# Kernel tuning notes

Hardware: AMD Instinct MI355X
Metric: run time of the kernel (lower is better)

## Reference

```python
import jax, jax.numpy as jnp
import numpy as np
import math

B, S, D, H = 2, 2048, 1024, 16
DH = D // H          # 64 head dim
BLK = 64             # SpargeAttn block size
TOPK = 0.5           # fraction of KV blocks kept per query block
NEG = -1e9


def setup_inputs() -> dict:
    key = jax.random.key(0)
    ks = jax.random.split(key, 8)
    s = 0.02
    return {
        "inputs": jax.random.normal(ks[0], (B, S, D), dtype=jnp.float32),
        "ln_g": jnp.ones((D,), jnp.float32),
        "ln_b": jnp.zeros((D,), jnp.float32),
        "Wq": jax.random.normal(ks[1], (D, D), jnp.float32) * s,
        "bq": jnp.zeros((D,), jnp.float32),
        "Wk": jax.random.normal(ks[2], (D, D), jnp.float32) * s,
        "bk": jnp.zeros((D,), jnp.float32),
        "Wv": jax.random.normal(ks[3], (D, D), jnp.float32) * s,
        "bv": jnp.zeros((D,), jnp.float32),
        "Wo": jax.random.normal(ks[4], (D, D), jnp.float32) * s,
        "bo": jnp.zeros((D,), jnp.float32),
    }


def _sparse_topk_attn(q, k, v):
    # q,k,v: [B,H,S,DH]. Block-mean-similarity top-k sparse causal attention
    # (SpargeAttn spas_sage2_attn_meansim_topk, fp32 reference semantics).
    nb = S // BLK
    qm = q.reshape(B, H, nb, BLK, DH).mean(3)          # [B,H,nb,DH]
    km = k.reshape(B, H, nb, BLK, DH).mean(3)
    sim = jnp.einsum('bhqd,bhkd->bhqk', qm, km)        # block similarity
    cblk = jnp.tril(jnp.ones((nb, nb), bool))          # causal block mask
    sim = jnp.where(cblk, sim, NEG)
    kk = max(1, int(math.ceil(TOPK * nb)))
    _, idx = jax.lax.top_k(sim, kk)                    # [B,H,nb,kk]
    blk = jax.nn.one_hot(idx, nb, dtype=jnp.float32).sum(-2) > 0  # [B,H,nb,nb]
    blk = (blk & cblk) | jnp.eye(nb, dtype=bool)       # keep diagonal block
    tok_mask = jnp.repeat(jnp.repeat(blk, BLK, axis=2), BLK, axis=3)  # [B,H,S,S]
    tok_mask = tok_mask & jnp.tril(jnp.ones((S, S), bool))
    scores = jnp.einsum('bhid,bhjd->bhij', q, k) / jnp.float32(math.sqrt(DH))
    scores = jnp.where(tok_mask, scores, NEG)
    p = jax.nn.softmax(scores, axis=-1)
    return jnp.einsum('bhij,bhjd->bhid', p, v)


def reference(inputs, ln_g, ln_b, Wq, bq, Wk, bk, Wv, bv, Wo, bo):
    # pre-norm LayerNorm
    mu = inputs.mean(-1, keepdims=True)
    var = inputs.var(-1, keepdims=True)
    x = (inputs - mu) * jax.lax.rsqrt(var + 1e-5) * ln_g + ln_b
    # QKV projections -> [B,H,S,DH]
    q = (x @ Wq + bq).reshape(B, S, H, DH).transpose(0, 2, 1, 3)
    k = (x @ Wk + bk).reshape(B, S, H, DH).transpose(0, 2, 1, 3)
    v = (x @ Wv + bv).reshape(B, S, H, DH).transpose(0, 2, 1, 3)
    ctx = _sparse_topk_attn(q, k, v)
    ctx = ctx.transpose(0, 2, 1, 3).reshape(B, S, D)
    return ctx @ Wo + bo
```

## Files before the change

### kernel.cpp

```cpp
#include <hip/hip_runtime.h>
#include <stdint.h>

#define DEV static __device__ __forceinline__

typedef __attribute__((ext_vector_type(8))) short s16x8;
typedef __attribute__((ext_vector_type(4))) float f32x4;

constexpr int Bdim = 2, Sdim = 2048, Ddim = 1024, Hdim = 16, DH = 64;
constexpr int Mrows = Bdim * Sdim;
constexpr int NB = 32;
constexpr int SEL_STRIDE = 18;

#define QSCALE 0.18033688011112042f
#define MFIX   8.0f

constexpr size_t OFF_XB    = 0;
constexpr size_t OFF_WTQKV = OFF_XB    + (size_t)Mrows*Ddim*2;
constexpr size_t OFF_WOT   = OFF_WTQKV + (size_t)3072*1024*2;
constexpr size_t OFF_QKV   = OFF_WOT   + (size_t)1024*1024*2;
constexpr size_t OFF_CTX   = OFF_QKV   + (size_t)Mrows*3072*2;
constexpr size_t OFF_XM    = OFF_CTX   + (size_t)Mrows*Ddim*2;
constexpr size_t OFF_QM    = OFF_XM    + (size_t)64*1024*4;
constexpr size_t OFF_KM    = OFF_QM    + (size_t)64*1024*4;
constexpr size_t OFF_BIASQ = OFF_KM    + (size_t)64*1024*4;
constexpr size_t OFF_SEL   = OFF_BIASQ + (size_t)3072*4;
constexpr size_t OFF_PART  = OFF_SEL   + (size_t)1024*SEL_STRIDE*4;

DEV float bf2f(unsigned short u){ union{unsigned int i; float f;} x; x.i = ((unsigned int)u)<<16; return x.f; }
DEV unsigned short f2bf(float f){ union{float f; unsigned int i;} x; x.f=f;
  unsigned int r = x.i + 0x7fffu + ((x.i>>16)&1u); return (unsigned short)(r>>16); }

DEV void gload16(const unsigned short* g, unsigned short* l){
  __builtin_amdgcn_global_load_lds(
      (__attribute__((address_space(1))) void*)(void*)g,
      (__attribute__((address_space(3))) void*)l, 16, 0, 0);
}

DEV unsigned int cvtpk(float a, float b){
  unsigned int r;
  asm("v_cvt_pk_bf16_f32 %0, %1, %2" : "=v"(r) : "v"(a), "v"(b));
  return r;
}

DEV float exp2fast(float x){
  float r;
  asm("v_exp_f32 %0, %1" : "=v"(r) : "v"(x));
  return r;
}

__global__ __launch_bounds__(256) void ln_kernel(const float* __restrict__ inp,
                                                 const float* __restrict__ gam,
                                                 const float* __restrict__ bet,
                                                 unsigned short* __restrict__ xb){
  const int row = blockIdx.x, t = threadIdx.x;
  __shared__ float red[8];
  const float4 v = ((const float4*)(inp + (size_t)row*Ddim))[t];
  float s  = v.x + v.y + v.z + v.w;
  float s2 = v.x*v.x + v.y*v.y + v.z*v.z + v.w*v.w;
#pragma unroll
  for (int mk=32; mk>=1; mk>>=1){ s += __shfl_xor(s, mk); s2 += __shfl_xor(s2, mk); }
  if ((t&63)==0){ red[t>>6] = s; red[4+(t>>6)] = s2; }
  __syncthreads();
  s  = red[0]+red[1]+red[2]+red[3];
  s2 = red[4]+red[5]+red[6]+red[7];
  const float mu  = s * (1.f/Ddim);
  const float var = s2 * (1.f/Ddim) - mu*mu;
  const float rs  = rsqrtf(var + 1e-5f);
  const float4 gv = ((const float4*)gam)[t];
  const float4 bv = ((const float4*)bet)[t];
  float o0 = (v.x-mu)*rs*gv.x + bv.x;
  float o1 = (v.y-mu)*rs*gv.y + bv.y;
  float o2 = (v.z-mu)*rs*gv.z + bv.z;
  float o3 = (v.w-mu)*rs*gv.w + bv.w;
  uint2 u;
  u.x = (unsigned int)f2bf(o0) | ((unsigned int)f2bf(o1)<<16);
  u.y = (unsigned int)f2bf(o2) | ((unsigned int)f2bf(o3)<<16);
  ((uint2*)(xb + (size_t)row*Ddim))[t] = u;
}

__global__ __launch_bounds__(256) void xm_kernel(const float* __restrict__ inp,
                                                 const float* __restrict__ gam,
                                                 const float* __restrict__ bet,
                                                 float* __restrict__ xm){
  const int blk = blockIdx.x, t = threadIdx.x;
  const int w = t>>6, lane = t&63;
  __shared__ float part[4][1024];
  float4 gv[4], bv[4];
#pragma unroll
  for (int p=0;p<4;++p){ gv[p] = ((const float4*)gam)[lane + 64*p];
                         bv[p] = ((const float4*)bet)[lane + 64*p]; }
  float ax[4][4];
#pragma unroll
  for (int p=0;p<4;++p)
#pragma unroll
    for (int c=0;c<4;++c) ax[p][c]=0.f;
  for (int rr=0; rr<16; ++rr){
    const int row = blk*64 + w*16 + rr;
    const float4* rp = (const float4*)(inp + (size_t)row*Ddim);
    float4 v[4]; float s=0.f, s2=0.f;
#pragma unroll
    for (int p=0;p<4;++p){
      v[p] = rp[lane + 64*p];
      s  += v[p].x+v[p].y+v[p].z+v[p].w;
      s2 += v[p].x*v[p].x+v[p].y*v[p].y+v[p].z*v[p].z+v[p].w*v[p].w;
    }
#pragma unroll
    for (int mk=32; mk>=1; mk>>=1){ s += __shfl_xor(s,mk); s2 += __shfl_xor(s2,mk); }
    const float mu = s*(1.f/Ddim);
    const float var = s2*(1.f/Ddim) - mu*mu;
    const float rs = rsqrtf(var + 1e-5f);
#pragma unroll
    for (int p=0;p<4;++p){
      ax[p][0] += (v[p].x-mu)*rs*gv[p].x + bv[p].x;
      ax[p][1] += (v[p].y-mu)*rs*gv[p].y + bv[p].y;
      ax[p][2] += (v[p].z-mu)*rs*gv[p].z + bv[p].z;
      ax[p][3] += (v[p].w-mu)*rs*gv[p].w + bv[p].w;
    }
  }
#pragma unroll
  for (int p=0;p<4;++p){
    float4 o; o.x=ax[p][0]; o.y=ax[p][1]; o.z=ax[p][2]; o.w=ax[p][3];
    ((float4*)&part[w][0])[lane + 64*p] = o;
  }
  __syncthreads();
  float4 r0 = ((float4*)&part[0][0])[t];
  float4 r1 = ((float4*)&part[1][0])[t];
  float4 r2 = ((float4*)&part[2][0])[t];
  float4 r3 = ((float4*)&part[3][0])[t];
  float4 o;
  o.x = (r0.x+r1.x+r2.x+r3.x)*(1.f/64);
  o.y = (r0.y+r1.y+r2.y+r3.y)*(1.f/64);
  o.z = (r0.z+r1.z+r2.z+r3.z)*(1.f/64);
  o.w = (r0.w+r1.w+r2.w+r3.w)*(1.f/64);
  ((float4*)(xm + (size_t)blk*Ddim))[t] = o;
}

__global__ __launch_bounds__(256) void wtrans4_kernel(const float* __restrict__ Wq,
                                                      const float* __restrict__ Wk,
                                                      const float* __restrict__ Wv,
                                                      const float* __restrict__ Wo,
                                                      const float* __restrict__ bq,
                                                      const float* __restrict__ bk,
                                                      const float* __restrict__ bv,
                                                      unsigned short* __restrict__ wtqkv,
                                                      unsigned short* __restrict__ wot,
                                                      float* __restrict__ bqkv){
  __shared__ float tile[32][33];
  const int z = blockIdx.z;
  const float* W = (z==0)?Wq:(z==1)?Wk:(z==2)?Wv:Wo;
  unsigned short* Wt = (z<3) ? (wtqkv + (size_t)z*1024*1024) : wot;
  const int n0 = blockIdx.x*32, k0 = blockIdx.y*32;
  const int t = threadIdx.x, r = t>>5, c = t&31;
  if (z<3 && blockIdx.x==0 && blockIdx.y==0){
    const float* bb = (z==0)?bq:(z==1)?bk:bv;
#pragma unroll
    for (int i=0;i<4;++i) bqkv[z*1024 + t + 256*i] = bb[t + 256*i];
  }
#pragma unroll
  for (int i=0;i<4;++i) tile[r+8*i][c] = W[(size_t)(k0 + r + 8*i)*1024 + n0 + c];
  __syncthreads();
  const int nr = t >> 3, kq = (t & 7) * 4;
  unsigned int w0 = (unsigned int)f2bf(tile[kq  ][nr]) | ((unsigned int)f2bf(tile[kq+1][nr])<<16);
  unsigned int w1 = (unsigned int)f2bf(tile[kq+2][nr]) | ((unsigned int)f2bf(tile[kq+3][nr])<<16);
  uint2 st; st.x = w0; st.y = w1;
  *(uint2*)&Wt[(size_t)(n0 + nr)*1024 + k0 + kq] = st;
}

__global__ __launch_bounds__(256) void qmkm_part(const float* __restrict__ xm,
    const float* __restrict__ Wq, const float* __restrict__ Wk,
    float* __restrict__ part){
  const int c  = blockIdx.x*256 + threadIdx.x;
  const int rg = blockIdx.y >> 3, ks = blockIdx.y & 7;
  const int z  = blockIdx.z;
  const float* W = z ? Wk : Wq;
  const int r0 = rg*16, k0 = ks*128;
  float acc[16];
#pragma unroll
  for (int r=0;r<16;++r) acc[r]=0.f;
  for (int k=0;k<128;k+=4){
    const float wv0 = W[(size_t)(k0+k  )*1024 + c];
    const float wv1 = W[(size_t)(k0+k+1)*1024 + c];
    const float wv2 = W[(size_t)(k0+k+2)*1024 + c];
    const float wv3 = W[(size_t)(k0+k+3)*1024 + c];
#pragma unroll
    for (int r=0;r<16;++r){
      const float4 xv = *(const float4*)&xm[(size_t)(r0+r)*1024 + k0 + k];
      acc[r] = fmaf(xv.w, wv3, fmaf(xv.z, wv2, fmaf(xv.y, wv1, fmaf(xv.x, wv0, acc[r]))));
    }
  }
  float* dst = part + (((size_t)z*8 + ks)*64 + r0)*1024 + c;
#pragma unroll
  for (int r=0;r<16;++r) dst[(size_t)r*1024] = acc[r];
}

__global__ __launch_bounds__(256) void qmkm_reduce(const float* __restrict__ part,
    const float* __restrict__ bq, const float* __restrict__ bk,
    float* __restrict__ qm, float* __restrict__ km){
  const int idx = blockIdx.x*256 + threadIdx.x;
  const int z = blockIdx.y;
  const int c = idx & 1023, r = idx >> 10;
  const float* p = part + ((size_t)z*8*64*1024) + (size_t)r*1024 + c;
  float s = 0.f;
#pragma unroll
  for (int ks=0; ks<8; ++ks) s += p[(size_t)ks*64*1024];
  s += z ? bk[c] : bq[c];
  (z ? km : qm)[(size_t)r*1024 + c] = s;
}

__global__ __launch_bounds__(256) void topk_kernel(const float* __restrict__ qm,
                                                   const float* __restrict__ km,
                                                   int* __restrict__ sel){
  const int bhq = blockIdx.x;
  const int qb = bhq & 31, h = (bhq>>5) & 15, b = bhq >> 9;
  const int t = threadIdx.x;
  __shared__ float sim[32];
  __shared__ int keep[32];
  const int kb = t>>3, l8 = t&7;
  float acc = 0.f;
  if (kb <= qb){
    const float* qv = qm + (size_t)(b*32 + qb)*1024 + h*64;
    const float* kv = km + (size_t)(b*32 + kb)*1024 + h*64;
#pragma unroll
    for (int d=0; d<8; ++d) acc += qv[l8*8+d] * kv[l8*8+d];
  }
  acc += __shfl_xor(acc,1); acc += __shfl_xor(acc,2); acc += __shfl_xor(acc,4);
  if (l8==0) sim[kb] = (kb<=qb) ? acc : -1e30f;
  __syncthreads();
  if (t < 32){
    int k2 = t; int ok = 0;
    if (k2 <= qb){
      float sv = sim[k2]; int rank = 0;
      for (int j=0;j<=qb;++j){
        float sj = sim[j];
        rank += (sj > sv) || (sj == sv && j < k2);
      }
      ok = (rank < 16) || (k2 == qb);
    }
    keep[t] = ok;
  }
  __syncthreads();
  if (t == 0){
    int* dstp = sel + (size_t)bhq * SEL_STRIDE;
    int c = 0;
    for (int j=0;j<32;++j) if (keep[j]) dstp[1+c++] = j;
    dstp[0] = c;
  }
}

#define G_STAGE(bsel, kofs) do { \
  gload16(A0 + (kofs), ldsA + (bsel)*4096 + (wid*2+0)*512); \
  gload16(A1 + (kofs), ldsA + (bsel)*4096 + (wid*2+1)*512); \
  gload16(B0 + (kofs), ldsB + (bsel)*4096 + (wid*2+0)*512); \
  gload16(B1 + (kofs), ldsB + (bsel)*4096 + (wid*2+1)*512); \
} while(0)

#define G_COMPUTE(bsel) do { \
  s16x8 af[4], bfr[4]; \
  _Pragma("unroll") \
  for (int mi=0;mi<4;++mi){ \
    int row = wr*64 + mi*16 + rl; \
    af[mi] = *(const s16x8*)((char*)ldsA + (bsel)*8192 + row*64 + ((g ^ ((row>>1)&3))<<4)); \
  } \
  _Pragma("unroll") \
  for (int ni=0;ni<4;++ni){ \
    int row = wc*64 + ni*16 + rl; \
    bfr[ni] = *(const s16x8*)((char*)ldsB + (bsel)*8192 + row*64 + ((g ^ ((row>>1)&3))<<4)); \
  } \
  _Pragma("unroll") \
  for (int mi=0;mi<4;++mi) \
    _Pragma("unroll") \
    for (int ni=0;ni<4;++ni) \
      acc[mi][ni] = __builtin_amdgcn_mfma_f32_16x16x32_bf16(af[mi], bfr[ni], acc[mi][ni], 0,0,0); \
} while(0)

template<int OUT_BF16, int SCALEQ>
__global__ __launch_bounds__(256) void gemm_bt(const unsigned short* __restrict__ A,
                                               const unsigned short* __restrict__ Bt,
                                               const float* __restrict__ bias,
                                               void* __restrict__ C, int N){
  constexpr int K = 1024;
  constexpr int NT = K/32;
  __shared__ unsigned short ldsA[3*128*32];
  __shared__ unsigned short ldsB[3*128*32];
  const int t = threadIdx.x, lane = t & 63, wid = t >> 6;
  const int wr = wid >> 1, wc = wid & 1;
  const int rl = lane & 15, g = lane >> 4;

  const int nbx = gridDim.x, nby = gridDim.y;
  const int id  = blockIdx.y * nbx + blockIdx.x;
  const int xcd = id & 7, j = id >> 3;
  const int MBP = nby >> 2, NBP = nbx >> 1;
  const int mg = xcd >> 1, ng = xcd & 1;
  const int m0 = (mg*MBP + (j % MBP)) * 128;
  const int n0 = (ng*NBP + (j / MBP)) * 128;

  const f32x4 ZERO4 = {0.f,0.f,0.f,0.f};
  f32x4 acc[4][4];
#pragma unroll
  for (int i=0;i<4;++i)
#pragma unroll
    for (int j2=0;j2<4;++j2) acc[i][j2] = ZERO4;

  const int slot0 = wid*128 + lane, slot1 = slot0 + 64;
  const int sr0 = slot0>>2, sc0 = slot0&3;
  const int sr1 = slot1>>2, sc1 = slot1&3;
  const unsigned short* A0 = A  + (size_t)(m0 + sr0)*K + (sc0 ^ ((sr0>>1)&3))*8;
  const unsigned short* A1 = A  + (size_t)(m0 + sr1)*K + (sc1 ^ ((sr1>>1)&3))*8;
  const unsigned short* B0 = Bt + (size_t)(n0 + sr0)*K + (sc0 ^ ((sr0>>1)&3))*8;
  const unsigned short* B1 = Bt + (size_t)(n0 + sr1)*K + (sc1 ^ ((sr1>>1)&3))*8;

  G_STAGE(0, 0);
  G_STAGE(1, 32);

  for (int ti=0; ti<NT; ++ti){
    const int cur = ti % 3;
    if (ti+2 < NT){
      G_STAGE((ti+2)%3, (ti+2)*32);
      asm volatile("s_waitcnt vmcnt(8)" ::: "memory");
    } else if (ti+1 < NT){
      asm volatile("s_waitcnt vmcnt(4)" ::: "memory");
    } else {
      asm volatile("s_waitcnt vmcnt(0)" ::: "memory");
    }
    __builtin_amdgcn_s_barrier();
    __builtin_amdgcn_sched_barrier(0);
    G_COMPUTE(cur);
    __builtin_amdgcn_sched_barrier(0);
    __builtin_amdgcn_s_barrier();
  }

  const int r4 = g*4;
#pragma unroll
  for (int mi=0;mi<4;++mi){
#pragma unroll
    for (int ni=0;ni<4;++ni){
      int col = n0 + wc*64 + ni*16 + rl;
      float bb = bias[col];
      float sc = (SCALEQ && col < 1024) ? QSCALE : 1.0f;
#pragma unroll
      for (int e=0;e<4;++e){
        int row = m0 + wr*64 + mi*16 + r4 + e;
        float v = (acc[mi][ni][e] + bb) * sc;
        if (OUT_BF16) ((unsigned short*)C)[(size_t)row*N + col] = f2bf(v);
        else          ((float*)C)[(size_t)row*N + col] = v;
      }
    }
  }
}

#define G64_STAGE(bsel, kofs) do { \
  gload16(A0 + (kofs), ldsA + (bsel)*4096 + (wid*2+0)*512); \
  gload16(A1 + (kofs), ldsA + (bsel)*4096 + (wid*2+1)*512); \
  gload16(B0 + (kofs), ldsB + (bsel)*2048 + wid*512); \
} while(0)

#define G64_COMPUTE(bsel) do { \
  s16x8 af[4], bfr[2]; \
  _Pragma("unroll") \
  for (int mi=0;mi<4;++mi){ \
    int row = wr*64 + mi*16 + rl; \
    af[mi] = *(const s16x8*)((char*)ldsA + (bsel)*8192 + row*64 + ((g ^ ((row>>1)&3))<<4)); \
  } \
  _Pragma("unroll") \
  for (int ni=0;ni<2;++ni){ \
    int row = wc*32 + ni*16 + rl; \
    bfr[ni] = *(const s16x8*)((char*)ldsB + (bsel)*4096 + row*64 + ((g ^ ((row>>1)&3))<<4)); \
  } \
  _Pragma("unroll") \
  for (int mi=0;mi<4;++mi) \
    _Pragma("unroll") \
    for (int ni=0;ni<2;++ni) \
      acc[mi][ni] = __builtin_amdgcn_mfma_f32_16x16x32_bf16(af[mi], bfr[ni], acc[mi][ni], 0,0,0); \
} while(0)

__global__ __launch_bounds__(256) void gemm_bt64(const unsigned short* __restrict__ A,
                                                 const unsigned short* __restrict__ Bt,
                                                 const float* __restrict__ bias,
                                                 float* __restrict__ C, int N){
  constexpr int K = 1024;
  constexpr int NT = K/32;
  __shared__ unsigned short ldsA[3*128*32];
  __shared__ unsigned short ldsB[3*64*32];
  const int t = threadIdx.x, lane = t & 63, wid = t >> 6;
  const int wr = wid >> 1, wc = wid & 1;
  const int rl = lane & 15, g = lane >> 4;

  const int id  = blockIdx.y * gridDim.x + blockIdx.x;
  const int xcd = id & 7, j = id >> 3;
  const int mg = xcd >> 1, ng = xcd & 1;
  const int m0 = (mg*8 + (j & 7)) * 128;
  const int n0 = (ng*8 + (j >> 3)) * 64;

  const f32x4 ZERO4 = {0.f,0.f,0.f,0.f};
  f32x4 acc[4][2];
#pragma unroll
  for (int i=0;i<4;++i)
#pragma unroll
    for (int j2=0;j2<2;++j2) acc[i][j2] = ZERO4;

  const int slot0 = wid*128 + lane, slot1 = slot0 + 64;
  const int sr0 = slot0>>2, sc0 = slot0&3;
  const int sr1 = slot1>>2, sc1 = slot1&3;
  const unsigned short* A0 = A + (size_t)(m0 + sr0)*K + (sc0 ^ ((sr0>>1)&3))*8;
  const unsigned short* A1 = A + (size_t)(m0 + sr1)*K + (sc1 ^ ((sr1>>1)&3))*8;
  const int slotB = wid*64 + lane;
  const int srB = slotB>>2, scB = slotB&3;
  const unsigned short* B0 = Bt + (size_t)(n0 + srB)*K + (scB ^ ((srB>>1)&3))*8;

  G64_STAGE(0, 0);
  G64_STAGE(1, 32);

  for (int ti=0; ti<NT; ++ti){
    const int cur = ti % 3;
    if (ti+2 < NT){
      G64_STAGE((ti+2)%3, (ti+2)*32);
      asm volatile("s_waitcnt vmcnt(6)" ::: "memory");
    } else if (ti+1 < NT){
      asm volatile("s_waitcnt vmcnt(3)" ::: "memory");
    } else {
      asm volatile("s_waitcnt vmcnt(0)" ::: "memory");
    }
    __builtin_amdgcn_s_barrier();
    __builtin_amdgcn_sched_barrier(0);
    G64_COMPUTE(cur);
    __builtin_amdgcn_sched_barrier(0);
    __builtin_amdgcn_s_barrier();
  }

  const int r4 = g*4;
#pragma unroll
  for (int mi=0;mi<4;++mi){
#pragma unroll
    for (int ni=0;ni<2;++ni){
      int col = n0 + wc*32 + ni*16 + rl;
      float bb = bias[col];
#pragma unroll
      for (int e=0;e<4;++e){
        int row = m0 + wr*64 + mi*16 + r4 + e;
        C[(size_t)row*N + col] = acc[mi][ni][e] + bb;
      }
    }
  }
}

__global__ __launch_bounds__(256) void attn_kernel(const unsigned short* __restrict__ qkv,
                                                   const int* __restrict__ sel,
                                                   unsigned short* __restrict__ ctx){
  const int id = blockIdx.x;
  const int xcd = id & 7, jj = id >> 3;
  const int bh = xcd + 8*(jj/24);
  const int tau = jj % 24;
  const int h = bh & 15, b = bh >> 4;
  int qbl[2]; int nq;
  if (tau < 8){ qbl[0]=tau; qbl[1]=15-tau; nq=2; }
  else        { qbl[0]=tau+8; qbl[1]=0;    nq=1; }

  const int t = threadIdx.x, wid = t >> 6, lane = t & 63;
  const int rl = lane & 15, g = lane >> 4;
  const int q_local = wid*16 + rl;

  __shared__ unsigned short K_s[2][4096];
  __shared__ unsigned short V_s[2][4096];

  const int jst = t >> 2, cq = t & 3;
  const int r2 = t >> 3, dq = t & 7;
  const unsigned short* kbase = qkv + (size_t)(b*Sdim + jst)*3072 + 1024 + h*DH + cq*16;
  const unsigned short* vbase = qkv + (size_t)(b*Sdim + 2*r2)*3072 + 2048 + h*DH + dq*8;
  const int kwb0 = jst*128 + (((cq*2  ) ^ (jst&7))<<4);
  const int kwb1 = jst*128 + (((cq*2+1) ^ (jst&7))<<4);
  const f32x4 ZERO4 = {0.f,0.f,0.f,0.f};

  const int src0 = (rl + 16*((2*g  ) & 3)) << 2;
  const int src1 = (rl + 16*((2*g+1) & 3)) << 2;
  const bool hsel = (g >> 1);

  for (int iq=0; iq<nq; ++iq){
    const int qb = qbl[iq];
    const int* selrow = sel + (size_t)(((b*Hdim)+h)*NB + qb) * SEL_STRIDE;
    const int ns = selrow[0];

    const int qg0 = b*Sdim + qb*64 + q_local;
    const unsigned short* qbase = qkv + (size_t)qg0*3072 + h*DH;
    s16x8 qa[2];
    qa[0] = *(const s16x8*)(qbase + g*8);
    qa[1] = *(const s16x8*)(qbase + 32 + g*8);

    f32x4 o[4];
    float l_p = 0.f;
#pragma unroll
    for (int f=0; f<4; ++f) o[f] = ZERO4;

    __syncthreads();

    int kb = selrow[1];
    s16x8 kr0, kr1, vr0, vr1;
    {
      const size_t off = (size_t)kb*64*3072;
      kr0 = *(const s16x8*)(kbase + off);
      kr1 = *(const s16x8*)(kbase + off + 8);
      vr0 = *(const s16x8*)(vbase + off);
      vr1 = *(const s16x8*)(vbase + off + 3072);
    }

    for (int it=0; it<ns; ++it){
      const int buf = it & 1;
      unsigned short* Kw = &K_s[buf][0];
      unsigned short* Vw = &V_s[buf][0];
      *(s16x8*)((char*)Kw + kwb0) = kr0;
      *(s16x8*)((char*)Kw + kwb1) = kr1;
#pragma unroll
      for (int e=0;e<8;++e){
        const int d1 = dq*8 + e;
        const int sw = (d1&7) ^ (d1>>3);
        const unsigned int pr = (unsigned int)(unsigned short)vr0[e]
                              | ((unsigned int)(unsigned short)vr1[e] << 16);
        *(unsigned int*)((char*)Vw + d1*128 + ((4*r2) ^ (sw<<4))) = pr;
      }
      const int kbcur = kb;
      if (it+1 < ns){
        kb = selrow[2+it];
        const size_t off = (size_t)kb*64*3072;
        kr0 = *(const s16x8*)(kbase + off);
        kr1 = *(const s16x8*)(kbase + off + 8);
        vr0 = *(const s16x8*)(vbase + off);
        vr1 = *(const s16x8*)(vbase + off + 3072);
      }
      __syncthreads();

      f32x4 sfT[4];
#pragma unroll
      for (int f=0;f<4;++f) sfT[f] = ZERO4;
      __builtin_amdgcn_s_setprio(1);
#pragma unroll
      for (int kk=0;kk<2;++kk){
#pragma unroll
        for (int f=0;f<4;++f){
          const int jr = f*16 + rl;
          s16x8 kf = *(const s16x8*)((char*)Kw + jr*128 + (((kk*4+g) ^ (jr&7))<<4));
          sfT[f] = __builtin_amdgcn_mfma_f32_16x16x32_bf16(kf, qa[kk], sfT[f], 0,0,0);
        }
      }
      __builtin_amdgcn_s_setprio(0);
      if (kbcur == qb){
#pragma unroll
        for (int f=0;f<4;++f)
#pragma unroll
          for (int e=0;e<4;++e){
            const int j2 = f*16 + g*4 + e;
            if (j2 > q_local) sfT[f][e] = -1e9f;
          }
      }
      {
        float rs = 0.f;
#pragma unroll
        for (int f=0;f<4;++f)
#pragma unroll
          for (int e=0;e<4;++e){
            const float p = exp2fast(sfT[f][e] - MFIX);
            sfT[f][e] = p; rs += p;
          }
        l_p += rs;
      }

      unsigned int plo[4], phi[4];
#pragma unroll
      for (int f=0;f<4;++f){
        plo[f] = cvtpk(sfT[f][0], sfT[f][1]);
        phi[f] = cvtpk(sfT[f][2], sfT[f][3]);
      }

#pragma unroll
      for (int kk=0;kk<2;++kk){
        const int f0 = 2*kk, f1 = 2*kk+1;
        unsigned int a0, b0, w0, w1, w2, w3;
        a0 = __builtin_amdgcn_ds_bpermute(src0, plo[f0]);
        b0 = __builtin_amdgcn_ds_bpermute(src0, plo[f1]);
        w0 = hsel ? b0 : a0;
        a0 = __builtin_amdgcn_ds_bpermute(src0, phi[f0]);
        b0 = __builtin_amdgcn_ds_bpermute(src0, phi[f1]);
        w1 = hsel ? b0 : a0;
        a0 = __builtin_amdgcn_ds_bpermute(src1, plo[f0]);
        b0 = __builtin_amdgcn_ds_bpermute(src1, plo[f1]);
        w2 = hsel ? b0 : a0;
        a0 = __builtin_amdgcn_ds_bpermute(src1, phi[f0]);
        b0 = __builtin_amdgcn_ds_bpermute(src1, phi[f1]);
        w3 = hsel ? b0 : a0;
        union { unsigned int u[4]; s16x8 v; } pfc;
        pfc.u[0] = w0; pfc.u[1] = w1; pfc.u[2] = w2; pfc.u[3] = w3;
        const s16x8 pf = pfc.v;
        __builtin_amdgcn_s_setprio(1);
#pragma unroll
        for (int f=0;f<4;++f){
          const int d = f*16 + rl;
          const int sw = (d&7) ^ (d>>3);
          s16x8 vf = *(const s16x8*)((char*)Vw + d*128 + ((64*kk + 16*g) ^ (sw<<4)));
          o[f] = __builtin_amdgcn_mfma_f32_16x16x32_bf16(vf, pf, o[f], 0,0,0);
        }
        __builtin_amdgcn_s_setprio(0);
      }
    }

    {
      float l_r = l_p;
      l_r += __shfl_xor(l_r, 16);
      l_r += __shfl_xor(l_r, 32);
      const float inv = 1.f / l_r;
      unsigned short* crow = ctx + (size_t)qg0*Ddim + h*DH;
#pragma unroll
      for (int f=0;f<4;++f){
        uint2 st;
        st.x = (unsigned int)f2bf(o[f][0]*inv) | ((unsigned int)f2bf(o[f][1]*inv)<<16);
        st.y = (unsigned int)f2bf(o[f][2]*inv) | ((unsigned int)f2bf(o[f][3]*inv)<<16);
        *(uint2*)(crow + f*16 + g*4) = st;
      }
    }
  }
}

extern "C" void kernel_launch(void* const* d_in, const int* in_sizes, int n_in,
                              void* d_out, int out_size, void* d_ws, size_t ws_size,
                              hipStream_t stream){
  (void)in_sizes; (void)n_in; (void)out_size; (void)ws_size;
  const float* inp  = (const float*)d_in[0];
  const float* ln_g = (const float*)d_in[1];
  const float* ln_b = (const float*)d_in[2];
  const float* Wq   = (const float*)d_in[3];
  const float* bq   = (const float*)d_in[4];
  const float* Wk   = (const float*)d_in[5];
  const float* bk   = (const float*)d_in[6];
  const float* Wv   = (const float*)d_in[7];
  const float* bv   = (const float*)d_in[8];
  const float* Wo   = (const float*)d_in[9];
  const float* bo   = (const float*)d_in[10];

  char* ws = (char*)d_ws;
  unsigned short* xb    = (unsigned short*)(ws + OFF_XB);
  unsigned short* wtqkv = (unsigned short*)(ws + OFF_WTQKV);
  unsigned short* wot   = (unsigned short*)(ws + OFF_WOT);
  unsigned short* qkvb  = (unsigned short*)(ws + OFF_QKV);
  unsigned short* ctx   = (unsigned short*)(ws + OFF_CTX);
  float* xm   = (float*)(ws + OFF_XM);
  float* qm   = (float*)(ws + OFF_QM);
  float* km   = (float*)(ws + OFF_KM);
  float* bqkv = (float*)(ws + OFF_BIASQ);
  int*   sel  = (int*)(ws + OFF_SEL);
  float* part = (float*)(ws + OFF_PART);

  ln_kernel<<<Mrows, 256, 0, stream>>>(inp, ln_g, ln_b, xb);
  xm_kernel<<<64, 256, 0, stream>>>(inp, ln_g, ln_b, xm);
  wtrans4_kernel<<<dim3(32,32,4), 256, 0, stream>>>(Wq, Wk, Wv, Wo, bq, bk, bv, wtqkv, wot, bqkv);
  qmkm_part<<<dim3(4,32,2), 256, 0, stream>>>(xm, Wq, Wk, part);
  qmkm_reduce<<<dim3(256,2), 256, 0, stream>>>(part, bq, bk, qm, km);
  topk_kernel<<<1024, 256, 0, stream>>>(qm, km, sel);
  gemm_bt<1,1><<<dim3(24,32), 256, 0, stream>>>(xb, wtqkv, bqkv, (void*)qkvb, 3072);
  attn_kernel<<<768, 256, 0, stream>>>(qkvb, sel, ctx);
  gemm_bt64<<<dim3(16,32), 256, 0, stream>>>(ctx, wot, bo, (float*)d_out, 1024);
}
```

Baseline: 140.0 us.

## Fuse LN, block-mean and weight transpose kernels; one query block per attention CTA

Merges the layernorm, block-mean and weight transpose/convert kernels into one prep kernel that picks its role from the block index, cutting two launches and letting the three jobs overlap on the GPU. The attention kernel now gives each CTA a single query block (1024 CTAs), launched with the heaviest causal query blocks first, replacing the old pairing of two query blocks per CTA. Finer work units may balance load better and shorten the tail, at the cost of more CTAs and less reuse of setup work. The fused prep kernel always reserves 16 KB of shared memory, which may lower occupancy for the layernorm blocks.

New measurement: 141.3 us. Within noise of the previous version (+0.9%).

```diff
diff --git a/kernel.cpp b/kernel.cpp
--- a/kernel.cpp
+++ b/kernel.cpp
@@ -48,122 +48,124 @@
   return r;
 }
 
-__global__ __launch_bounds__(256) void ln_kernel(const float* __restrict__ inp,
-                                                 const float* __restrict__ gam,
-                                                 const float* __restrict__ bet,
-                                                 unsigned short* __restrict__ xb){
-  const int row = blockIdx.x, t = threadIdx.x;
-  __shared__ float red[8];
-  const float4 v = ((const float4*)(inp + (size_t)row*Ddim))[t];
-  float s  = v.x + v.y + v.z + v.w;
-  float s2 = v.x*v.x + v.y*v.y + v.z*v.z + v.w*v.w;
-#pragma unroll
-  for (int mk=32; mk>=1; mk>>=1){ s += __shfl_xor(s, mk); s2 += __shfl_xor(s2, mk); }
-  if ((t&63)==0){ red[t>>6] = s; red[4+(t>>6)] = s2; }
-  __syncthreads();
-  s  = red[0]+red[1]+red[2]+red[3];
-  s2 = red[4]+red[5]+red[6]+red[7];
-  const float mu  = s * (1.f/Ddim);
-  const float var = s2 * (1.f/Ddim) - mu*mu;
-  const float rs  = rsqrtf(var + 1e-5f);
-  const float4 gv = ((const float4*)gam)[t];
-  const float4 bv = ((const float4*)bet)[t];
-  float o0 = (v.x-mu)*rs*gv.x + bv.x;
-  float o1 = (v.y-mu)*rs*gv.y + bv.y;
-  float o2 = (v.z-mu)*rs*gv.z + bv.z;
-  float o3 = (v.w-mu)*rs*gv.w + bv.w;
-  uint2 u;
-  u.x = (unsigned int)f2bf(o0) | ((unsigned int)f2bf(o1)<<16);
-  u.y = (unsigned int)f2bf(o2) | ((unsigned int)f2bf(o3)<<16);
-  ((uint2*)(xb + (size_t)row*Ddim))[t] = u;
-}
-
-__global__ __launch_bounds__(256) void xm_kernel(const float* __restrict__ inp,
-                                                 const float* __restrict__ gam,
-                                                 const float* __restrict__ bet,
-                                                 float* __restrict__ xm){
-  const int blk = blockIdx.x, t = threadIdx.x;
-  const int w = t>>6, lane = t&63;
-  __shared__ float part[4][1024];
-  float4 gv[4], bv[4];
-#pragma unroll
-  for (int p=0;p<4;++p){ gv[p] = ((const float4*)gam)[lane + 64*p];
-                         bv[p] = ((const float4*)bet)[lane + 64*p]; }
-  float ax[4][4];
-#pragma unroll
-  for (int p=0;p<4;++p)
-#pragma unroll
-    for (int c=0;c<4;++c) ax[p][c]=0.f;
-  for (int rr=0; rr<16; ++rr){
-    const int row = blk*64 + w*16 + rr;
-    const float4* rp = (const float4*)(inp + (size_t)row*Ddim);
-    float4 v[4]; float s=0.f, s2=0.f;
+__global__ __launch_bounds__(256) void prep_kernel(const float* __restrict__ inp,
+                                                   const float* __restrict__ gam,
+                                                   const float* __restrict__ bet,
+                                                   const float* __restrict__ Wq,
+                                                   const float* __restrict__ Wk,
+                                                   const float* __restrict__ Wv,
+                                                   const float* __restrict__ Wo,
+                                                   const float* __restrict__ bq,
+                                                   const float* __restrict__ bk,
+                                                   const float* __restrict__ bv,
+                                                   unsigned short* __restrict__ xb,
+                                                   float* __restrict__ xm,
+                                                   unsigned short* __restrict__ wtqkv,
+                                                   unsigned short* __restrict__ wot,
+                                                   float* __restrict__ bqkv){
+  __shared__ float sh[4][1024];
+  const int bid = blockIdx.x;
+  const int t = threadIdx.x;
+
+  if (bid < 4096){
+    const int row = bid;
+    float* red = &sh[0][0];
+    const float4 v = ((const float4*)(inp + (size_t)row*Ddim))[t];
+    float s  = v.x + v.y + v.z + v.w;
+    float s2 = v.x*v.x + v.y*v.y + v.z*v.z + v.w*v.w;
+#pragma unroll
+    for (int mk=32; mk>=1; mk>>=1){ s += __shfl_xor(s, mk); s2 += __shfl_xor(s2, mk); }
+    if ((t&63)==0){ red[t>>6] = s; red[4+(t>>6)] = s2; }
+    __syncthreads();
+    s  = red[0]+red[1]+red[2]+red[3];
+    s2 = red[4]+red[5]+red[6]+red[7];
+    const float mu  = s * (1.f/Ddim);
+    const float var = s2 * (1.f/Ddim) - mu*mu;
+    const float rs  = rsqrtf(var + 1e-5f);
+    const float4 gv = ((const float4*)gam)[t];
+    const float4 bv2 = ((const float4*)bet)[t];
+    float o0 = (v.x-mu)*rs*gv.x + bv2.x;
+    float o1 = (v.y-mu)*rs*gv.y + bv2.y;
+    float o2 = (v.z-mu)*rs*gv.z + bv2.z;
+    float o3 = (v.w-mu)*rs*gv.w + bv2.w;
+    uint2 u;
+    u.x = (unsigned int)f2bf(o0) | ((unsigned int)f2bf(o1)<<16);
+    u.y = (unsigned int)f2bf(o2) | ((unsigned int)f2bf(o3)<<16);
+    ((uint2*)(xb + (size_t)row*Ddim))[t] = u;
+  } else if (bid < 4160){
+    const int blk = bid - 4096;
+    const int w = t>>6, lane = t&63;
+    float4 gv[4], bvv[4];
+#pragma unroll
+    for (int p=0;p<4;++p){ gv[p] = ((const float4*)gam)[lane + 64*p];
+                           bvv[p] = ((const float4*)bet)[lane + 64*p]; }
+    float ax[4][4];
+#pragma unroll
+    for (int p=0;p<4;++p)
+#pragma unroll
+      for (int c=0;c<4;++c) ax[p][c]=0.f;
+    for (int rr=0; rr<16; ++rr){
+      const int row = blk*64 + w*16 + rr;
+      const float4* rp = (const float4*)(inp + (size_t)row*Ddim);
+      float4 v[4]; float s=0.f, s2=0.f;
+#pragma unroll
+      for (int p=0;p<4;++p){
+        v[p] = rp[lane + 64*p];
+        s  += v[p].x+v[p].y+v[p].z+v[p].w;
+        s2 += v[p].x*v[p].x+v[p].y*v[p].y+v[p].z*v[p].z+v[p].w*v[p].w;
+      }
+#pragma unroll
+      for (int mk=32; mk>=1; mk>>=1){ s += __shfl_xor(s,mk); s2 += __shfl_xor(s2,mk); }
+      const float mu = s*(1.f/Ddim);
+      const float var = s2*(1.f/Ddim) - mu*mu;
+      const float rs = rsqrtf(var + 1e-5f);
+#pragma unroll
+      for (int p=0;p<4;++p){
+        ax[p][0] += (v[p].x-mu)*rs*gv[p].x + bvv[p].x;
+        ax[p][1] += (v[p].y-mu)*rs*gv[p].y + bvv[p].y;
+        ax[p][2] += (v[p].z-mu)*rs*gv[p].z + bvv[p].z;
+        ax[p][3] += (v[p].w-mu)*rs*gv[p].w + bvv[p].w;
+      }
+    }
 #pragma unroll
     for (int p=0;p<4;++p){
-      v[p] = rp[lane + 64*p];
-      s  += v[p].x+v[p].y+v[p].z+v[p].w;
-      s2 += v[p].x*v[p].x+v[p].y*v[p].y+v[p].z*v[p].z+v[p].w*v[p].w;
-    }
-#pragma unroll
-    for (int mk=32; mk>=1; mk>>=1){ s += __shfl_xor(s,mk); s2 += __shfl_xor(s2,mk); }
-    const float mu = s*(1.f/Ddim);
-    const float var = s2*(1.f/Ddim) - mu*mu;
-    const float rs = rsqrtf(var + 1e-5f);
-#pragma unroll
-    for (int p=0;p<4;++p){
-      ax[p][0] += (v[p].x-mu)*rs*gv[p].x + bv[p].x;
-      ax[p][1] += (v[p].y-mu)*rs*gv[p].y + bv[p].y;
-      ax[p][2] += (v[p].z-mu)*rs*gv[p].z + bv[p].z;
-      ax[p][3] += (v[p].w-mu)*rs*gv[p].w + bv[p].w;
-    }
-  }
-#pragma unroll
-  for (int p=0;p<4;++p){
-    float4 o; o.x=ax[p][0]; o.y=ax[p][1]; o.z=ax[p][2]; o.w=ax[p][3];
-    ((float4*)&part[w][0])[lane + 64*p] = o;
-  }
-  __syncthreads();
-  float4 r0 = ((float4*)&part[0][0])[t];
-  float4 r1 = ((float4*)&part[1][0])[t];
-  float4 r2 = ((float4*)&part[2][0])[t];
-  float4 r3 = ((float4*)&part[3][0])[t];
-  float4 o;
-  o.x = (r0.x+r1.x+r2.x+r3.x)*(1.f/64);
-  o.y = (r0.y+r1.y+r2.y+r3.y)*(1.f/64);
-  o.z = (r0.z+r1.z+r2.z+r3.z)*(1.f/64);
-  o.w = (r0.w+r1.w+r2.w+r3.w)*(1.f/64);
-  ((float4*)(xm + (size_t)blk*Ddim))[t] = o;
-}
-
-__global__ __launch_bounds__(256) void wtrans4_kernel(const float* __restrict__ Wq,
-                                                      const float* __restrict__ Wk,
-                                                      const float* __restrict__ Wv,
-                                                      const float* __restrict__ Wo,
-                                                      const float* __restrict__ bq,
-                                                      const float* __restrict__ bk,
-                                                      const float* __restrict__ bv,
-                                                      unsigned short* __restrict__ wtqkv,
-                                                      unsigned short* __restrict__ wot,
-                                                      float* __restrict__ bqkv){
-  __shared__ float tile[32][33];
-  const int z = blockIdx.z;
-  const float* W = (z==0)?Wq:(z==1)?Wk:(z==2)?Wv:Wo;
-  unsigned short* Wt = (z<3) ? (wtqkv + (size_t)z*1024*1024) : wot;
-  const int n0 = blockIdx.x*32, k0 = blockIdx.y*32;
-  const int t = threadIdx.x, r = t>>5, c = t&31;
-  if (z<3 && blockIdx.x==0 && blockIdx.y==0){
-    const float* bb = (z==0)?bq:(z==1)?bk:bv;
-#pragma unroll
-    for (int i=0;i<4;++i) bqkv[z*1024 + t + 256*i] = bb[t + 256*i];
-  }
-#pragma unroll
-  for (int i=0;i<4;++i) tile[r+8*i][c] = W[(size_t)(k0 + r + 8*i)*1024 + n0 + c];
-  __syncthreads();
-  const int nr = t >> 3, kq = (t & 7) * 4;
-  unsigned int w0 = (unsigned int)f2bf(tile[kq  ][nr]) | ((unsigned int)f2bf(tile[kq+1][nr])<<16);
-  unsigned int w1 = (unsigned int)f2bf(tile[kq+2][nr]) | ((unsigned int)f2bf(tile[kq+3][nr])<<16);
-  uint2 st; st.x = w0; st.y = w1;
-  *(uint2*)&Wt[(size_t)(n0 + nr)*1024 + k0 + kq] = st;
+      float4 o; o.x=ax[p][0]; o.y=ax[p][1]; o.z=ax[p][2]; o.w=ax[p][3];
+      ((float4*)&sh[w][0])[lane + 64*p] = o;
+    }
+    __syncthreads();
+    float4 r0 = ((float4*)&sh[0][0])[t];
+    float4 r1 = ((float4*)&sh[1][0])[t];
+    float4 r2 = ((float4*)&sh[2][0])[t];
+    float4 r3 = ((float4*)&sh[3][0])[t];
+    float4 o;
+    o.x = (r0.x+r1.x+r2.x+r3.x)*(1.f/64);
+    o.y = (r0.y+r1.y+r2.y+r3.y)*(1.f/64);
+    o.z = (r0.z+r1.z+r2.z+r3.z)*(1.f/64);
+    o.w = (r0.w+r1.w+r2.w+r3.w)*(1.f/64);
+    ((float4*)(xm + (size_t)blk*Ddim))[t] = o;
+  } else {
+    const int wt = bid - 4160;
+    const int z = wt >> 10, rem = wt & 1023;
+    const int bx = rem & 31, by = rem >> 5;
+    const float* W = (z==0)?Wq:(z==1)?Wk:(z==2)?Wv:Wo;
+    unsigned short* Wt = (z<3) ? (wtqkv + (size_t)z*1024*1024) : wot;
+    const int n0 = bx*32, k0 = by*32;
+    const int r = t>>5, c = t&31;
+    float (*tile)[33] = (float(*)[33])&sh[0][0];
+    if (z<3 && bx==0 && by==0){
+      const float* bb = (z==0)?bq:(z==1)?bk:bv;
+#pragma unroll
+      for (int i=0;i<4;++i) bqkv[z*1024 + t + 256*i] = bb[t + 256*i];
+    }
+#pragma unroll
+    for (int i=0;i<4;++i) tile[r+8*i][c] = W[(size_t)(k0 + r + 8*i)*1024 + n0 + c];
+    __syncthreads();
+    const int nr = t >> 3, kq = (t & 7) * 4;
+    unsigned int w0 = (unsigned int)f2bf(tile[kq  ][nr]) | ((unsigned int)f2bf(tile[kq+1][nr])<<16);
+    unsigned int w1 = (unsigned int)f2bf(tile[kq+2][nr]) | ((unsigned int)f2bf(tile[kq+3][nr])<<16);
+    uint2 st; st.x = w0; st.y = w1;
+    *(uint2*)&Wt[(size_t)(n0 + nr)*1024 + k0 + kq] = st;
+  }
 }
 
 __global__ __launch_bounds__(256) void qmkm_part(const float* __restrict__ xm,
@@ -448,12 +450,9 @@
                                                    unsigned short* __restrict__ ctx){
   const int id = blockIdx.x;
   const int xcd = id & 7, jj = id >> 3;
-  const int bh = xcd + 8*(jj/24);
-  const int tau = jj % 24;
+  const int bh = xcd + 8*(jj >> 5);
+  const int qb = 31 - (jj & 31);
   const int h = bh & 15, b = bh >> 4;
-  int qbl[2]; int nq;
-  if (tau < 8){ qbl[0]=tau; qbl[1]=15-tau; nq=2; }
-  else        { qbl[0]=tau+8; qbl[1]=0;    nq=1; }
 
   const int t = threadIdx.x, wid = t >> 6, lane = t & 63;
   const int rl = lane & 15, g = lane >> 4;
@@ -474,145 +473,140 @@
   const int src1 = (rl + 16*((2*g+1) & 3)) << 2;
   const bool hsel = (g >> 1);
 
-  for (int iq=0; iq<nq; ++iq){
-    const int qb = qbl[iq];
-    const int* selrow = sel + (size_t)(((b*Hdim)+h)*NB + qb) * SEL_STRIDE;
-    const int ns = selrow[0];
-
-    const int qg0 = b*Sdim + qb*64 + q_local;
-    const unsigned short* qbase = qkv + (size_t)qg0*3072 + h*DH;
-    s16x8 qa[2];
-    qa[0] = *(const s16x8*)(qbase + g*8);
-    qa[1] = *(const s16x8*)(qbase + 32 + g*8);
-
-    f32x4 o[4];
-    float l_p = 0.f;
-#pragma unroll
-    for (int f=0; f<4; ++f) o[f] = ZERO4;
-
-    __syncthreads();
-
-    int kb = selrow[1];
-    s16x8 kr0, kr1, vr0, vr1;
-    {
+  const int* selrow = sel + (size_t)(((b*Hdim)+h)*NB + qb) * SEL_STRIDE;
+  const int ns = selrow[0];
+
+  const int qg0 = b*Sdim + qb*64 + q_local;
+  const unsigned short* qbase = qkv + (size_t)qg0*3072 + h*DH;
+  s16x8 qa[2];
+  qa[0] = *(const s16x8*)(qbase + g*8);
+  qa[1] = *(const s16x8*)(qbase + 32 + g*8);
+
+  f32x4 o[4];
+  float l_p = 0.f;
+#pragma unroll
+  for (int f=0; f<4; ++f) o[f] = ZERO4;
+
+  int kb = selrow[1];
+  s16x8 kr0, kr1, vr0, vr1;
+  {
+    const size_t off = (size_t)kb*64*3072;
+    kr0 = *(const s16x8*)(kbase + off);
+    kr1 = *(const s16x8*)(kbase + off + 8);
+    vr0 = *(const s16x8*)(vbase + off);
+    vr1 = *(const s16x8*)(vbase + off + 3072);
+  }
+
+  for (int it=0; it<ns; ++it){
+    const int buf = it & 1;
+    unsigned short* Kw = &K_s[buf][0];
+    unsigned short* Vw = &V_s[buf][0];
+    *(s16x8*)((char*)Kw + kwb0) = kr0;
+    *(s16x8*)((char*)Kw + kwb1) = kr1;
+#pragma unroll
+    for (int e=0;e<8;++e){
+      const int d1 = dq*8 + e;
+      const int sw = (d1&7) ^ (d1>>3);
+      const unsigned int pr = (unsigned int)(unsigned short)vr0[e]
+                            | ((unsigned int)(unsigned short)vr1[e] << 16);
+      *(unsigned int*)((char*)Vw + d1*128 + ((4*r2) ^ (sw<<4))) = pr;
+    }
+    const int kbcur = kb;
+    if (it+1 < ns){
+      kb = selrow[2+it];
       const size_t off = (size_t)kb*64*3072;
       kr0 = *(const s16x8*)(kbase + off);
       kr1 = *(const s16x8*)(kbase + off + 8);
       vr0 = *(const s16x8*)(vbase + off);
       vr1 = *(const s16x8*)(vbase + off + 3072);
     }
-
-    for (int it=0; it<ns; ++it){
-      const int buf = it & 1;
-      unsigned short* Kw = &K_s[buf][0];
-      unsigned short* Vw = &V_s[buf][0];
-      *(s16x8*)((char*)Kw + kwb0) = kr0;
-      *(s16x8*)((char*)Kw + kwb1) = kr1;
-#pragma unroll
-      for (int e=0;e<8;++e){
-        const int d1 = dq*8 + e;
-        const int sw = (d1&7) ^ (d1>>3);
-        const unsigned int pr = (unsigned int)(unsigned short)vr0[e]
-                              | ((unsigned int)(unsigned short)vr1[e] << 16);
-        *(unsigned int*)((char*)Vw + d1*128 + ((4*r2) ^ (sw<<4))) = pr;
+    __syncthreads();
+
+    f32x4 sfT[4];
+#pragma unroll
+    for (int f=0;f<4;++f) sfT[f] = ZERO4;
+    __builtin_amdgcn_s_setprio(1);
+#pragma unroll
+    for (int kk=0;kk<2;++kk){
+#pragma unroll
+      for (int f=0;f<4;++f){
+        const int jr = f*16 + rl;
+        s16x8 kf = *(const s16x8*)((char*)Kw + jr*128 + (((kk*4+g) ^ (jr&7))<<4));
+        sfT[f] = __builtin_amdgcn_mfma_f32_16x16x32_bf16(kf, qa[kk], sfT[f], 0,0,0);
       }
-      const int kbcur = kb;
-      if (it+1 < ns){
-        kb = selrow[2+it];
-        const size_t off = (size_t)kb*64*3072;
-        kr0 = *(const s16x8*)(kbase + off);
-        kr1 = *(const s16x8*)(kbase + off + 8);
-        vr0 = *(const s16x8*)(vbase + off);
-        vr1 = *(const s16x8*)(vbase + off + 3072);
-      }
-      __syncthreads();
-
-      f32x4 sfT[4];
-#pragma unroll
-      for (int f=0;f<4;++f) sfT[f] = ZERO4;
+    }
+    __builtin_amdgcn_s_setprio(0);
+    if (kbcur == qb){
+#pragma unroll
+      for (int f=0;f<4;++f)
+#pragma unroll
+        for (int e=0;e<4;++e){
+          const int j2 = f*16 + g*4 + e;
+          if (j2 > q_local) sfT[f][e] = -1e9f;
+        }
+    }
+    {
+      float rs = 0.f;
+#pragma unroll
+      for (int f=0;f<4;++f)
+#pragma unroll
+        for (int e=0;e<4;++e){
+          const float p = exp2fast(sfT[f][e] - MFIX);
+          sfT[f][e] = p; rs += p;
+        }
+      l_p += rs;
+    }
+
+    unsigned int plo[4], phi[4];
+#pragma unroll
+    for (int f=0;f<4;++f){
+      plo[f] = cvtpk(sfT[f][0], sfT[f][1]);
+      phi[f] = cvtpk(sfT[f][2], sfT[f][3]);
+    }
+
+#pragma unroll
+    for (int kk=0;kk<2;++kk){
+      const int f0 = 2*kk, f1 = 2*kk+1;
+      unsigned int a0, b0, w0, w1, w2, w3;
+      a0 = __builtin_amdgcn_ds_bpermute(src0, plo[f0]);
+      b0 = __builtin_amdgcn_ds_bpermute(src0, plo[f1]);
+      w0 = hsel ? b0 : a0;
+      a0 = __builtin_amdgcn_ds_bpermute(src0, phi[f0]);
+      b0 = __builtin_amdgcn_ds_bpermute(src0, phi[f1]);
+      w1 = hsel ? b0 : a0;
+      a0 = __builtin_amdgcn_ds_bpermute(src1, plo[f0]);
+      b0 = __builtin_amdgcn_ds_bpermute(src1, plo[f1]);
+      w2 = hsel ? b0 : a0;
+      a0 = __builtin_amdgcn_ds_bpermute(src1, phi[f0]);
+      b0 = __builtin_amdgcn_ds_bpermute(src1, phi[f1]);
+      w3 = hsel ? b0 : a0;
+      union { unsigned int u[4]; s16x8 v; } pfc;
+      pfc.u[0] = w0; pfc.u[1] = w1; pfc.u[2] = w2; pfc.u[3] = w3;
+      const s16x8 pf = pfc.v;
       __builtin_amdgcn_s_setprio(1);
 #pragma unroll
-      for (int kk=0;kk<2;++kk){
-#pragma unroll
-        for (int f=0;f<4;++f){
-          const int jr = f*16 + rl;
-          s16x8 kf = *(const s16x8*)((char*)Kw + jr*128 + (((kk*4+g) ^ (jr&7))<<4));
-          sfT[f] = __builtin_amdgcn_mfma_f32_16x16x32_bf16(kf, qa[kk], sfT[f], 0,0,0);
-        }
+      for (int f=0;f<4;++f){
+        const int d = f*16 + rl;
+        const int sw = (d&7) ^ (d>>3);
+        s16x8 vf = *(const s16x8*)((char*)Vw + d*128 + ((64*kk + 16*g) ^ (sw<<4)));
+        o[f] = __builtin_amdgcn_mfma_f32_16x16x32_bf16(vf, pf, o[f], 0,0,0);
       }
       __builtin_amdgcn_s_setprio(0);
-      if (kbcur == qb){
-#pragma unroll
-        for (int f=0;f<4;++f)
-#pragma unroll
-          for (int e=0;e<4;++e){
-            const int j2 = f*16 + g*4 + e;
-            if (j2 > q_local) sfT[f][e] = -1e9f;
-          }
-      }
-      {
-        float rs = 0.f;
-#pragma unroll
-        for (int f=0;f<4;++f)
-#pragma unroll
-          for (int e=0;e<4;++e){
-            const float p = exp2fast(sfT[f][e] - MFIX);
-            sfT[f][e] = p; rs += p;
-          }
-        l_p += rs;
-      }
-
-      unsigned int plo[4], phi[4];
-#pragma unroll
-      for (int f=0;f<4;++f){
-        plo[f] = cvtpk(sfT[f][0], sfT[f][1]);
-        phi[f] = cvtpk(sfT[f][2], sfT[f][3]);
-      }
-
-#pragma unroll
-      for (int kk=0;kk<2;++kk){
-        const int f0 = 2*kk, f1 = 2*kk+1;
-        unsigned int a0, b0, w0, w1, w2, w3;
-        a0 = __builtin_amdgcn_ds_bpermute(src0, plo[f0]);
-        b0 = __builtin_amdgcn_ds_bpermute(src0, plo[f1]);
-        w0 = hsel ? b0 : a0;
-        a0 = __builtin_amdgcn_ds_bpermute(src0, phi[f0]);
-        b0 = __builtin_amdgcn_ds_bpermute(src0, phi[f1]);
-        w1 = hsel ? b0 : a0;
-        a0 = __builtin_amdgcn_ds_bpermute(src1, plo[f0]);
-        b0 = __builtin_amdgcn_ds_bpermute(src1, plo[f1]);
-        w2 = hsel ? b0 : a0;
-        a0 = __builtin_amdgcn_ds_bpermute(src1, phi[f0]);
-        b0 = __builtin_amdgcn_ds_bpermute(src1, phi[f1]);
-        w3 = hsel ? b0 : a0;
-        union { unsigned int u[4]; s16x8 v; } pfc;
-        pfc.u[0] = w0; pfc.u[1] = w1; pfc.u[2] = w2; pfc.u[3] = w3;
-        const s16x8 pf = pfc.v;
-        __builtin_amdgcn_s_setprio(1);
-#pragma unroll
-        for (int f=0;f<4;++f){
-          const int d = f*16 + rl;
-          const int sw = (d&7) ^ (d>>3);
-          s16x8 vf = *(const s16x8*)((char*)Vw + d*128 + ((64*kk + 16*g) ^ (sw<<4)));
-          o[f] = __builtin_amdgcn_mfma_f32_16x16x32_bf16(vf, pf, o[f], 0,0,0);
-        }
-        __builtin_amdgcn_s_setprio(0);
-      }
-    }
-
-    {
-      float l_r = l_p;
-      l_r += __shfl_xor(l_r, 16);
-      l_r += __shfl_xor(l_r, 32);
-      const float inv = 1.f / l_r;
-      unsigned short* crow = ctx + (size_t)qg0*Ddim + h*DH;
-#pragma unroll
-      for (int f=0;f<4;++f){
-        uint2 st;
-        st.x = (unsigned int)f2bf(o[f][0]*inv) | ((unsigned int)f2bf(o[f][1]*inv)<<16);
-        st.y = (unsigned int)f2bf(o[f][2]*inv) | ((unsigned int)f2bf(o[f][3]*inv)<<16);
-        *(uint2*)(crow + f*16 + g*4) = st;
-      }
+    }
+  }
+
+  {
+    float l_r = l_p;
+    l_r += __shfl_xor(l_r, 16);
+    l_r += __shfl_xor(l_r, 32);
+    const float inv = 1.f / l_r;
+    unsigned short* crow = ctx + (size_t)qg0*Ddim + h*DH;
+#pragma unroll
+    for (int f=0;f<4;++f){
+      uint2 st;
+      st.x = (unsigned int)f2bf(o[f][0]*inv) | ((unsigned int)f2bf(o[f][1]*inv)<<16);
+      st.y = (unsigned int)f2bf(o[f][2]*inv) | ((unsigned int)f2bf(o[f][3]*inv)<<16);
+      *(uint2*)(crow + f*16 + g*4) = st;
     }
   }
 }
@@ -646,13 +640,12 @@
   int*   sel  = (int*)(ws + OFF_SEL);
   float* part = (float*)(ws + OFF_PART);
 
-  ln_kernel<<<Mrows, 256, 0, stream>>>(inp, ln_g, ln_b, xb);
-  xm_kernel<<<64, 256, 0, stream>>>(inp, ln_g, ln_b, xm);
-  wtrans4_kernel<<<dim3(32,32,4), 256, 0, stream>>>(Wq, Wk, Wv, Wo, bq, bk, bv, wtqkv, wot, bqkv);
+  prep_kernel<<<8256, 256, 0, stream>>>(inp, ln_g, ln_b, Wq, Wk, Wv, Wo,
+                                        bq, bk, bv, xb, xm, wtqkv, wot, bqkv);
   qmkm_part<<<dim3(4,32,2), 256, 0, stream>>>(xm, Wq, Wk, part);
   qmkm_reduce<<<dim3(256,2), 256, 0, stream>>>(part, bq, bk, qm, km);
   topk_kernel<<<1024, 256, 0, stream>>>(qm, km, sel);
   gemm_bt<1,1><<<dim3(24,32), 256, 0, stream>>>(xb, wtqkv, bqkv, (void*)qkvb, 3072);
-  attn_kernel<<<768, 256, 0, stream>>>(qkvb, sel, ctx);
+  attn_kernel<<<1024, 256, 0, stream>>>(qkvb, sel, ctx);
   gemm_bt64<<<dim3(16,32), 256, 0, stream>>>(ctx, wot, bo, (float*)d_out, 1024);
 }
```
